# Kernel optimization log

Hardware: AMD Instinct MI355X
Metric: run time of the kernel (lower is better)

The kernel has to match this reference:

```python
import jax, jax.numpy as jnp
import numpy as np

B = 4096
FEAT = 512
EMB = 64
HID = 1024
NUM_CLASSES = 64   # == option_num == noise_lib_Y.shape[0]
LIB_X = 256
LIB_Y = 256
OUT_J = 256


def setup_inputs() -> dict:
    key = jax.random.key(0)
    ks = jax.random.split(key, 16)
    s = lambda k, shape, fan: jax.random.normal(k, shape, jnp.float32) / np.sqrt(fan)
    d_in = FEAT + EMB
    return {
        "state": jax.random.normal(ks[0], (B, FEAT), jnp.float32),
        "option": jax.random.randint(ks[1], (B,), 0, NUM_CLASSES, jnp.int64),
        "embed_table": s(ks[2], (NUM_CLASSES, EMB), EMB),
        "Wx1": s(ks[3], (d_in, HID), d_in), "bx1": jnp.zeros((HID,), jnp.float32),
        "Wx2": s(ks[4], (HID, LIB_X), HID), "bx2": jnp.zeros((LIB_X,), jnp.float32),
        "Wy1": s(ks[5], (d_in, HID), d_in), "by1": jnp.zeros((HID,), jnp.float32),
        "Wy2": s(ks[6], (HID, LIB_Y), HID), "by2": jnp.zeros((LIB_Y,), jnp.float32),
        "noise_lib_X": s(ks[7], (LIB_X, OUT_J), LIB_X),
        "noise_lib_Y": s(ks[8], (NUM_CLASSES, LIB_Y, OUT_J), LIB_Y),
    }


def _mlp(x, W1, b1, W2, b2):
    # MLP_RELU, layer_num=2: Linear -> ReLU -> Linear
    h = jax.nn.relu(x @ W1 + b1)
    return h @ W2 + b2


def reference(state, option, embed_table, Wx1, bx1, Wx2, bx2,
              Wy1, by1, Wy2, by2, noise_lib_X, noise_lib_Y):
    option_embed = embed_table[option]                      # [B, EMB]
    all_state = jnp.concatenate([state, option_embed], axis=-1)
    cls_X = _mlp(all_state, Wx1, bx1, Wx2, bx2)             # [B, LIB_X]
    cls_Y = _mlp(all_state, Wy1, by1, Wy2, by2)             # [B, LIB_Y]
    # Original: einsum('bi,mij->bmj') then mask with one_hot(option).
    # Mathematically identical gather-then-matmul (honors the routing sparsity):
    noise_Y_sel = noise_lib_Y[option]                       # [B, LIB_Y, OUT_J]
    generate_noise_Y = jnp.einsum('bi,bij->bj', cls_Y, noise_Y_sel)
    generate_noise_X = cls_X @ noise_lib_X                  # [B, OUT_J]
    return (generate_noise_X, generate_noise_Y)
```

## Files before the change

### kernel.cpp

```cpp
#include <hip/hip_runtime.h>

typedef unsigned short u16;
typedef unsigned int u32;

using f32x4  = __attribute__((ext_vector_type(4))) float;
using bf16x8 = __attribute__((ext_vector_type(8))) __bf16;

#define DEV __device__ __forceinline__

DEV u16 f2bf(float f) {
  union { float f; u32 u; } x; x.f = f;
  return (u16)((x.u + 0x7fffu + ((x.u >> 16) & 1u)) >> 16);
}
DEV float bf2f(u16 h) {
  union { u32 u; float f; } x; x.u = ((u32)h) << 16;
  return x.f;
}

DEV void async_cp16(const u16* g, u16* l) {
  __builtin_amdgcn_global_load_lds((const __attribute__((address_space(1))) void*)g,
                                   (__attribute__((address_space(3))) void*)l,
                                   16, 0, 0);
}

static constexpr int BATCH = 4096;
static constexpr int FEAT  = 512;
static constexpr int EMB   = 64;
static constexpr int HID   = 1024;
static constexpr int NC    = 64;
static constexpr int DIN   = 576;
static constexpr int LIB   = 256;

DEV void detect_lite(const u32* __restrict__ sraw, const u32* __restrict__ oraw,
                     int* isf32, int* ostr) {
  __shared__ int cib, conz;
  const int t = threadIdx.x;
  if (t == 0) { cib = 0; conz = 0; }
  u32 w = sraw[t];
  u32 e = (w >> 7) & 0xFFu;
  unsigned long long m1 = __ballot(e >= 100 && e <= 142);
  unsigned long long m2 = __ballot((t & 1) && oraw[t] != 0);
  __syncthreads();
  if ((t & 63) == 0) {
    atomicAdd(&cib, __popcll(m1));
    atomicAdd(&conz, __popcll(m2));
  }
  __syncthreads();
  *isf32 = (cib < 128) ? 1 : 0;
  *ostr  = (conz == 0) ? 2 : 1;
}

DEV void load16_bf(u16* v, const void* __restrict__ in, size_t off, int isf32) {
  if (isf32) {
    const float4* s = (const float4*)((const float*)in + off);
    float4 a0 = s[0], a1 = s[1], a2 = s[2], a3 = s[3];
    v[0] = f2bf(a0.x); v[1] = f2bf(a0.y); v[2]  = f2bf(a0.z); v[3]  = f2bf(a0.w);
    v[4] = f2bf(a1.x); v[5] = f2bf(a1.y); v[6]  = f2bf(a1.z); v[7]  = f2bf(a1.w);
    v[8] = f2bf(a2.x); v[9] = f2bf(a2.y); v[10] = f2bf(a2.z); v[11] = f2bf(a2.w);
    v[12] = f2bf(a3.x); v[13] = f2bf(a3.y); v[14] = f2bf(a3.z); v[15] = f2bf(a3.w);
  } else {
    const uint4* s = (const uint4*)((const u16*)in + off);
    *(uint4*)&v[0] = s[0];
    *(uint4*)&v[8] = s[1];
  }
}

DEV void do_transpose64(u16* lds, const void* __restrict__ in,
                        u16* __restrict__ out, int R, int C,
                        int by, int bx, int isf32) {
  u16* tile = lds;
  const int t = threadIdx.x;
  {
    const int r = t >> 2, c0 = (t & 3) * 16;
    u16 v[16];
    load16_bf(v, in, (size_t)(by * 64 + r) * C + (bx * 64 + c0), isf32);
    *(uint4*)&tile[r * 72 + c0]     = *(uint4*)&v[0];
    *(uint4*)&tile[r * 72 + c0 + 8] = *(uint4*)&v[8];
  }
  __syncthreads();
  {
    const int c = t & 63, rs = (t >> 6) * 16;
    u16 w[16];
#pragma unroll
    for (int i = 0; i < 16; ++i) w[i] = tile[(rs + i) * 72 + c];
    size_t oo = (size_t)(bx * 64 + c) * R + (by * 64 + rs);
    *(uint4*)&out[oo]     = *(uint4*)&w[0];
    *(uint4*)&out[oo + 8] = *(uint4*)&w[8];
  }
}

DEV void tgemm_task(u16* lds, const void* __restrict__ nX,
                    const void* __restrict__ Wx2, u16* __restrict__ T,
                    int mt, int nt, int isf32) {
  u16* Als = lds;
  u16* Bls = lds + 64 * 72;
  const int t = threadIdx.x;
  const int m0 = mt * 64, q0 = nt * 64;
  const int lane = t & 63, wid = t >> 6;
  const int wm = wid >> 1, wn = wid & 1;
  const int lr = lane & 15, lq = lane >> 4;
  f32x4 acc[2][2] = {};
  for (int k0 = 0; k0 < LIB; k0 += 64) {
    __syncthreads();
    {
      const int r = t >> 2, c0 = (t & 3) * 16;
      u16 v[16];
      load16_bf(v, nX, (size_t)(k0 + r) * LIB + m0 + c0, isf32);
#pragma unroll
      for (int j = 0; j < 16; ++j) Als[(c0 + j) * 72 + r] = v[j];
      const int q = t >> 2, ic = (t & 3) * 16;
      u16 w16[16];
      load16_bf(w16, Wx2, (size_t)(q0 + q) * LIB + k0 + ic, isf32);
      u16* dst = &Bls[((ic >> 5) * 64 + q) * 32 + (ic & 31)];
      *(uint4*)dst       = *(uint4*)&w16[0];
      *(uint4*)(dst + 8) = *(uint4*)&w16[8];
    }
    __syncthreads();
#pragma unroll
    for (int sl = 0; sl < 2; ++sl) {
      bf16x8 av[2], bv[2];
#pragma unroll
      for (int i2 = 0; i2 < 2; ++i2)
        av[i2] = *(const bf16x8*)&Als[(wm * 32 + i2 * 16 + lr) * 72 + sl * 32 + lq * 8];
#pragma unroll
      for (int j2 = 0; j2 < 2; ++j2)
        bv[j2] = *(const bf16x8*)&Bls[(sl * 64 + wn * 32 + j2 * 16 + lr) * 32 + lq * 8];
#pragma unroll
      for (int i2 = 0; i2 < 2; ++i2)
#pragma unroll
        for (int j2 = 0; j2 < 2; ++j2)
          acc[i2][j2] = __builtin_amdgcn_mfma_f32_16x16x32_bf16(av[i2], bv[j2], acc[i2][j2], 0, 0, 0);
    }
  }
#pragma unroll
  for (int j2 = 0; j2 < 2; ++j2) {
    const int gc = q0 + wn * 32 + j2 * 16 + lr;
#pragma unroll
    for (int i2 = 0; i2 < 2; ++i2) {
      const int gr = m0 + wm * 32 + i2 * 16 + lq * 4;
#pragma unroll
      for (int r = 0; r < 4; ++r)
        T[(size_t)(gr + r) * HID + gc] = f2bf(acc[i2][j2][r]);
    }
  }
}

struct PrepArgs {
  const void *state, *emb, *Wx1, *Wy1;
  const int* opt;
  u16 *all_state, *WT1x, *WT1y;
};
static constexpr int PB_CONCAT = BATCH * 36 / 256;
static constexpr int PB_WT1 = (DIN / 64) * (HID / 64);
static constexpr int PREP_BLOCKS = PB_CONCAT + 2 * PB_WT1;

__global__ __launch_bounds__(256) void prep_k(PrepArgs a) {
  __shared__ __align__(16) u16 plds[64 * 72];
  int isf32, os;
  detect_lite((const u32*)a.state, (const u32*)a.opt, &isf32, &os);
  int bid = blockIdx.x;
  const int t = threadIdx.x;
  if (bid < PB_CONCAT) {
    int idx = bid * 256 + t;
    int b = idx / 36, ch = idx % 36;
    const void* base;
    size_t srcoff;
    if (ch < 32) { base = a.state; srcoff = (size_t)b * FEAT + ch * 16; }
    else {
      base = a.emb;
      srcoff = (size_t)a.opt[(size_t)b * os] * EMB + (ch - 32) * 16;
    }
    u16 o[16];
    load16_bf(o, base, srcoff, isf32);
    u16* dst = a.all_state + (size_t)b * DIN + ch * 16;
    *(uint4*)dst       = *(const uint4*)&o[0];
    *(uint4*)(dst + 8) = *(const uint4*)&o[8];
    return;
  }
  bid -= PB_CONCAT;
  if (bid < PB_WT1) { do_transpose64(plds, a.Wx1, a.WT1x, DIN, HID, bid >> 4, bid & 15, isf32); return; }
  bid -= PB_WT1;
  do_transpose64(plds, a.Wy1, a.WT1y, DIN, HID, bid >> 4, bid & 15, isf32);
}

template <int BM, int BN, int SLABS, bool RELU>
DEV void gemm_tile(u16* lds, const u16* __restrict__ A, const u16* __restrict__ Bt,
                   const void* bias, void* C, int N, int K, int m0, int n0,
                   int isf32, bool cf32, bool bf32) {
  constexpr int WM = BM / 2, WN = BN / 2, TM = WM / 16, TN = WN / 16;
  u16* As = lds;
  u16* Bs = lds + BM * 32 * SLABS;
  const int t = threadIdx.x;
  const int lane = t & 63, wid = t >> 6;
  const int wm = wid >> 1, wn = wid & 1;
  const int lr = lane & 15, lq = lane >> 4;
  f32x4 acc[TM][TN] = {};
  for (int k0 = 0; k0 < K; k0 += 32 * SLABS) {
    __syncthreads();
#pragma unroll
    for (int sl = 0; sl < SLABS; ++sl) {
#pragma unroll
      for (int u = 0; u < BM / 64; ++u) {
        int unit = u * 256 + t;
        int r = unit >> 2, c8 = (unit & 3) * 8;
        async_cp16(A + (size_t)(m0 + r) * K + (k0 + sl * 32 + c8),
                   &As[(sl * BM + r) * 32 + c8]);
      }
#pragma unroll
      for (int u = 0; u < BN / 64; ++u) {
        int unit = u * 256 + t;
        int r = unit >> 2, c8 = (unit & 3) * 8;
        async_cp16(Bt + (size_t)(n0 + r) * K + (k0 + sl * 32 + c8),
                   &Bs[(sl * BN + r) * 32 + c8]);
      }
    }
    __syncthreads();
#pragma unroll
    for (int sl = 0; sl < SLABS; ++sl) {
      bf16x8 av[TM], bv[TN];
#pragma unroll
      for (int i = 0; i < TM; ++i)
        av[i] = *(const bf16x8*)&As[(sl * BM + wm * WM + i * 16 + lr) * 32 + lq * 8];
#pragma unroll
      for (int j = 0; j < TN; ++j)
        bv[j] = *(const bf16x8*)&Bs[(sl * BN + wn * WN + j * 16 + lr) * 32 + lq * 8];
#pragma unroll
      for (int i = 0; i < TM; ++i)
#pragma unroll
        for (int j = 0; j < TN; ++j)
          acc[i][j] = __builtin_amdgcn_mfma_f32_16x16x32_bf16(av[i], bv[j], acc[i][j], 0, 0, 0);
    }
  }
#pragma unroll
  for (int j = 0; j < TN; ++j) {
    const int gc = n0 + wn * WN + j * 16 + lr;
    const float bval = bias
        ? (bf32 ? ((const float*)bias)[gc] : bf2f(((const u16*)bias)[gc]))
        : 0.f;
#pragma unroll
    for (int i = 0; i < TM; ++i) {
      const int gr = m0 + wm * WM + i * 16 + lq * 4;
#pragma unroll
      for (int r = 0; r < 4; ++r) {
        float v = acc[i][j][r] + bval;
        if (RELU) v = fmaxf(v, 0.f);
        const size_t idx = (size_t)(gr + r) * N + gc;
        if (cf32) ((float*)C)[idx] = v;
        else      ((u16*)C)[idx] = f2bf(v);
      }
    }
  }
}

struct G1Args {
  const u16 *all_state, *WT1x, *WT1y;
  const void *bx1, *by1, *Wy2, *nX, *Wx2, *bx2, *state, *opt;
  u16 *h_x, *h_y, *WT2y, *T;
  float* b2x;
};
static constexpr int G1_GEMM = 1024;
static constexpr int G1_BLOCKS = G1_GEMM + 64 + 64 + 4;

__global__ __launch_bounds__(256) void gemm1_k(G1Args a) {
  __shared__ __align__(16) u16 lds[(128 + 64) * 96];
  __shared__ float red[4][64];
  int isf32, os;
  detect_lite((const u32*)a.state, (const u32*)a.opt, &isf32, &os);
  int bid = blockIdx.x;
  const int t = threadIdx.x;
  if (bid < G1_GEMM) {
    const int v = (bid & 7) * 128 + (bid >> 3);
    const int x = v & 15, y = (v >> 4) & 31, z = v >> 9;
    gemm_tile<128, 64, 3, true>(lds,
        a.all_state, z ? a.WT1y : a.WT1x, z ? a.by1 : a.bx1,
        z ? a.h_y : a.h_x, HID, DIN, y * 128, x * 64, isf32, false, isf32);
    return;
  }
  bid -= G1_GEMM;
  if (bid < 64) { do_transpose64(lds, a.Wy2, a.WT2y, HID, LIB, bid >> 2, bid & 3, isf32); return; }
  bid -= 64;
  if (bid < 64) { tgemm_task(lds, a.nX, a.Wx2, a.T, bid & 3, bid >> 2, isf32); return; }
  bid -= 64;
  {
    const int j = bid * 64 + (t & 63), g = t >> 6;
    float acc = 0.f;
    for (int ii = 0; ii < 64; ++ii) {
      const int i = g * 64 + ii;
      float s = isf32 ? ((const float*)a.bx2)[i] : bf2f(((const u16*)a.bx2)[i]);
      float v = isf32 ? ((const float*)a.nX)[(size_t)i * LIB + j]
                      : bf2f(((const u16*)a.nX)[(size_t)i * LIB + j]);
      acc += s * v;
    }
    red[g][t & 63] = acc;
    __syncthreads();
    if (g == 0)
      a.b2x[j] = red[0][t & 63] + red[1][t & 63] + red[2][t & 63] + red[3][t & 63];
  }
}

struct GArg { const u16* A; const u16* Bt; const void* bias; void* C; int cflag; int bflag; };

template <int BM, int BN, int SLABS, bool RELU>
__global__ __launch_bounds__(256) void gemm_bt(GArg g0, GArg g1, int N, int K,
                                               const void* state, const void* opt) {
  __shared__ __align__(16) u16 lds[(BM + BN) * 32 * SLABS];
  int isf32, os;
  detect_lite((const u32*)state, (const u32*)opt, &isf32, &os);
  const int cpx = gridDim.x >> 3;
  const int v = (blockIdx.x & 7) * cpx + (blockIdx.x >> 3);
  const int nx = N / BN, my = BATCH / BM;
  const int x = v % nx;
  const int rem = v / nx;
  const int y = rem % my, z = rem / my;
  const GArg g = z ? g1 : g0;
  gemm_tile<BM, BN, SLABS, RELU>(lds, g.A, g.Bt, g.bias, g.C, N, K,
                                 y * BM, x * BN,
                                 isf32, g.cflag && isf32, g.bflag || isf32);
}

struct TailArgs {
  const u16* cls_y;
  const void *nY, *state;
  const int* opt;
  void* out;
};

static constexpr int TSTR = 266;

__global__ __launch_bounds__(256) void tail_k(TailArgs a) {
  __shared__ __align__(16) u16 lds[25216];
  __shared__ int lcnt;
  int isf32, os;
  detect_lite((const u32*)a.state, (const u32*)a.opt, &isf32, &os);
  const bool of32 = (isf32 != 0);
  const int t = threadIdx.x;
  const int lane = t & 63, w = t >> 6, lr = lane & 15, lq = lane >> 4;

  u16* Bts  = lds;
  u16* Asm  = lds + 64 * TSTR;
  u16* list = lds + 80 * TSTR;
  const int v = (blockIdx.x & 7) * 64 + (blockIdx.x >> 3);
  const int m = v >> 3;
  const int n0 = ((v >> 1) & 3) * 64;
  const int half = v & 1;
  if (t == 0) lcnt = 0;

#pragma unroll
  for (int pass = 0; pass < 4; ++pass) {
    const int k = pass * 64 + (t >> 2), nc = (t & 3) * 16;
    u16 vv[16];
    load16_bf(vv, a.nY, ((size_t)m * LIB + k) * LIB + n0 + nc, isf32);
#pragma unroll
    for (int j = 0; j < 16; ++j) Bts[(nc + j) * TSTR + k] = vv[j];
  }

  __syncthreads();
  const int bstart = half * (BATCH / 2), bend = bstart + BATCH / 2;
  for (int base = bstart; base < bend; base += 256) {
    const int b = base + t;
    const int e = a.opt[(size_t)b * os];
    unsigned long long mk = __ballot(e == m);
    const int nw = __popcll(mk);
    int wbase = 0;
    if (lane == 0 && nw) wbase = atomicAdd(&lcnt, nw);
    wbase = __shfl(wbase, 0);
    const int mypre = __popcll(mk & ((1ull << lane) - 1ull));
    if (e == m) list[wbase + mypre] = (u16)b;
  }
  __syncthreads();
  const int cnt = lcnt;
  const size_t out_off = (size_t)BATCH * LIB;

  for (int ch = 0; ch < cnt; ch += 16) {
    __syncthreads();
    {
      const int r = t >> 4, cb = (t & 15) * 16;
      if (ch + r < cnt) {
        const u16* src = a.cls_y + (size_t)list[ch + r] * LIB + cb;
        *(uint4*)&Asm[r * TSTR + cb]     = *(const uint4*)src;
        *(uint4*)&Asm[r * TSTR + cb + 8] = *(const uint4*)(src + 8);
      } else {
        uint4 z{0, 0, 0, 0};
        *(uint4*)&Asm[r * TSTR + cb]     = z;
        *(uint4*)&Asm[r * TSTR + cb + 8] = z;
      }
    }
    __syncthreads();
    f32x4 acc = {};
#pragma unroll
    for (int kk = 0; kk < LIB; kk += 32) {
      bf16x8 av = *(const bf16x8*)&Asm[lr * TSTR + kk + lq * 8];
      bf16x8 bv = *(const bf16x8*)&Bts[(w * 16 + lr) * TSTR + kk + lq * 8];
      acc = __builtin_amdgcn_mfma_f32_16x16x32_bf16(av, bv, acc, 0, 0, 0);
    }
#pragma unroll
    for (int r = 0; r < 4; ++r) {
      const int rowc = lq * 4 + r;
      if (ch + rowc < cnt) {
        const size_t oi = out_off + (size_t)list[ch + rowc] * LIB
                        + (n0 + w * 16 + lr);
        if (of32) ((float*)a.out)[oi] = acc[r];
        else      ((u16*)a.out)[oi] = f2bf(acc[r]);
      }
    }
  }
}

extern "C" void kernel_launch(void* const* d_in, const int* in_sizes, int n_in,
                              void* d_out, int out_size, void* d_ws, size_t ws_size,
                              hipStream_t stream) {
  char* p = (char*)d_ws;
  auto alloc = [&](size_t bytes) { char* r = p; p += (bytes + 255) & ~(size_t)255; return r; };
  u16* all_state = (u16*)alloc((size_t)BATCH * DIN * 2);
  u16* h_x   = (u16*)alloc((size_t)BATCH * HID * 2);
  u16* h_y   = (u16*)alloc((size_t)BATCH * HID * 2);
  u16* cls_y = (u16*)alloc((size_t)BATCH * LIB * 2);
  u16* WT1x  = (u16*)alloc((size_t)HID * DIN * 2);
  u16* WT1y  = (u16*)alloc((size_t)HID * DIN * 2);
  u16* WT2y  = (u16*)alloc((size_t)LIB * HID * 2);
  u16* T     = (u16*)alloc((size_t)LIB * HID * 2);
  float* b2x = (float*)alloc((size_t)LIB * 4);

  const void* state = d_in[0];
  const void* opt   = d_in[1];

  PrepArgs pa;
  pa.state = state; pa.opt = (const int*)opt; pa.emb = d_in[2];
  pa.Wx1 = d_in[3]; pa.Wy1 = d_in[7];
  pa.all_state = all_state; pa.WT1x = WT1x; pa.WT1y = WT1y;
  prep_k<<<PREP_BLOCKS, 256, 0, stream>>>(pa);

  G1Args g1;
  g1.all_state = all_state; g1.WT1x = WT1x; g1.WT1y = WT1y;
  g1.bx1 = d_in[4]; g1.by1 = d_in[8];
  g1.Wy2 = d_in[9]; g1.nX = d_in[11]; g1.Wx2 = d_in[5]; g1.bx2 = d_in[6];
  g1.state = state; g1.opt = opt;
  g1.h_x = h_x; g1.h_y = h_y; g1.WT2y = WT2y; g1.T = T; g1.b2x = b2x;
  gemm1_k<<<G1_BLOCKS, 256, 0, stream>>>(g1);

  GArg g2x{h_x, T, b2x, d_out, 1, 1};
  GArg g2y{h_y, WT2y, d_in[10], cls_y, 0, 0};
  gemm_bt<64, 64, 4, false><<<512, 256, 0, stream>>>(
      g2x, g2y, LIB, HID, state, opt);

  TailArgs ta{cls_y, d_in[12], state, (const int*)opt, d_out};
  tail_k<<<512, 256, 0, stream>>>(ta);
}
```

Before: 151.4 us.

## Fuse all stages into one persistent kernel with grid-wide barriers

Replaces the four separate launches (prep, first GEMM, second GEMM, routed tail) with one 512-block, 512-thread kernel. The stages are separated by atomic-counter grid barriers, which are reset with a memset before launch. Each block is split into two 256-thread halves that work on independent tiles, and the first-layer GEMM slab count drops from 3 to 2. This removes inter-kernel launch gaps and drain time. In exchange it depends on all 512 blocks being co-resident to avoid deadlock, and it leaves half the threads idle in the second GEMM and tail stages.

```diff
diff --git a/kernel.cpp b/kernel.cpp
--- a/kernel.cpp
+++ b/kernel.cpp
@@ -30,6 +30,17 @@
 static constexpr int NC    = 64;
 static constexpr int DIN   = 576;
 static constexpr int LIB   = 256;
+static constexpr int NBLK  = 512;
+
+DEV void gbar(int* bar) {
+  __syncthreads();
+  if (threadIdx.x == 0) {
+    __hip_atomic_fetch_add(bar, 1, __ATOMIC_ACQ_REL, __HIP_MEMORY_SCOPE_AGENT);
+    while (__hip_atomic_load(bar, __ATOMIC_ACQUIRE, __HIP_MEMORY_SCOPE_AGENT) < NBLK)
+      __builtin_amdgcn_s_sleep(2);
+  }
+  __syncthreads();
+}
 
 DEV void detect_lite(const u32* __restrict__ sraw, const u32* __restrict__ oraw,
                      int* isf32, int* ostr) {
@@ -46,7 +57,7 @@
     atomicAdd(&conz, __popcll(m2));
   }
   __syncthreads();
-  *isf32 = (cib < 128) ? 1 : 0;
+  *isf32 = (cib < (int)(blockDim.x >> 1)) ? 1 : 0;
   *ostr  = (conz == 0) ? 2 : 1;
 }
 
@@ -65,13 +76,11 @@
   }
 }
 
-DEV void do_transpose64(u16* lds, const void* __restrict__ in,
+DEV void do_transpose64(u16* tile, const void* __restrict__ in,
                         u16* __restrict__ out, int R, int C,
-                        int by, int bx, int isf32) {
-  u16* tile = lds;
-  const int t = threadIdx.x;
-  {
-    const int r = t >> 2, c0 = (t & 3) * 16;
+                        int by, int bx, int isf32, int tt) {
+  {
+    const int r = tt >> 2, c0 = (tt & 3) * 16;
     u16 v[16];
     load16_bf(v, in, (size_t)(by * 64 + r) * C + (bx * 64 + c0), isf32);
     *(uint4*)&tile[r * 72 + c0]     = *(uint4*)&v[0];
@@ -79,7 +88,7 @@
   }
   __syncthreads();
   {
-    const int c = t & 63, rs = (t >> 6) * 16;
+    const int c = tt & 63, rs = (tt >> 6) * 16;
     u16 w[16];
 #pragma unroll
     for (int i = 0; i < 16; ++i) w[i] = tile[(rs + i) * 72 + c];
@@ -89,29 +98,27 @@
   }
 }
 
-DEV void tgemm_task(u16* lds, const void* __restrict__ nX,
+DEV void tgemm_task(u16* L, const void* __restrict__ nX,
                     const void* __restrict__ Wx2, u16* __restrict__ T,
-                    int mt, int nt, int isf32) {
-  u16* Als = lds;
-  u16* Bls = lds + 64 * 72;
-  const int t = threadIdx.x;
+                    int mt, int nt, int isf32, int tt) {
+  u16* Als = L;
+  u16* Bls = L + 64 * 72;
   const int m0 = mt * 64, q0 = nt * 64;
-  const int lane = t & 63, wid = t >> 6;
+  const int lane = tt & 63, wid = tt >> 6;
   const int wm = wid >> 1, wn = wid & 1;
   const int lr = lane & 15, lq = lane >> 4;
   f32x4 acc[2][2] = {};
   for (int k0 = 0; k0 < LIB; k0 += 64) {
     __syncthreads();
     {
-      const int r = t >> 2, c0 = (t & 3) * 16;
+      const int r = tt >> 2, c0 = (tt & 3) * 16;
       u16 v[16];
       load16_bf(v, nX, (size_t)(k0 + r) * LIB + m0 + c0, isf32);
 #pragma unroll
       for (int j = 0; j < 16; ++j) Als[(c0 + j) * 72 + r] = v[j];
-      const int q = t >> 2, ic = (t & 3) * 16;
       u16 w16[16];
-      load16_bf(w16, Wx2, (size_t)(q0 + q) * LIB + k0 + ic, isf32);
-      u16* dst = &Bls[((ic >> 5) * 64 + q) * 32 + (ic & 31)];
+      load16_bf(w16, Wx2, (size_t)(q0 + r) * LIB + k0 + c0, isf32);
+      u16* dst = &Bls[((c0 >> 5) * 64 + r) * 32 + (c0 & 31)];
       *(uint4*)dst       = *(uint4*)&w16[0];
       *(uint4*)(dst + 8) = *(uint4*)&w16[8];
     }
@@ -145,262 +152,248 @@
   }
 }
 
-struct PrepArgs {
-  const void *state, *emb, *Wx1, *Wy1;
-  const int* opt;
-  u16 *all_state, *WT1x, *WT1y;
-};
-static constexpr int PB_CONCAT = BATCH * 36 / 256;
-static constexpr int PB_WT1 = (DIN / 64) * (HID / 64);
-static constexpr int PREP_BLOCKS = PB_CONCAT + 2 * PB_WT1;
-
-__global__ __launch_bounds__(256) void prep_k(PrepArgs a) {
-  __shared__ __align__(16) u16 plds[64 * 72];
-  int isf32, os;
-  detect_lite((const u32*)a.state, (const u32*)a.opt, &isf32, &os);
-  int bid = blockIdx.x;
-  const int t = threadIdx.x;
-  if (bid < PB_CONCAT) {
-    int idx = bid * 256 + t;
-    int b = idx / 36, ch = idx % 36;
-    const void* base;
-    size_t srcoff;
-    if (ch < 32) { base = a.state; srcoff = (size_t)b * FEAT + ch * 16; }
-    else {
-      base = a.emb;
-      srcoff = (size_t)a.opt[(size_t)b * os] * EMB + (ch - 32) * 16;
-    }
-    u16 o[16];
-    load16_bf(o, base, srcoff, isf32);
-    u16* dst = a.all_state + (size_t)b * DIN + ch * 16;
-    *(uint4*)dst       = *(const uint4*)&o[0];
-    *(uint4*)(dst + 8) = *(const uint4*)&o[8];
-    return;
-  }
-  bid -= PB_CONCAT;
-  if (bid < PB_WT1) { do_transpose64(plds, a.Wx1, a.WT1x, DIN, HID, bid >> 4, bid & 15, isf32); return; }
-  bid -= PB_WT1;
-  do_transpose64(plds, a.Wy1, a.WT1y, DIN, HID, bid >> 4, bid & 15, isf32);
-}
-
 template <int BM, int BN, int SLABS, bool RELU>
-DEV void gemm_tile(u16* lds, const u16* __restrict__ A, const u16* __restrict__ Bt,
-                   const void* bias, void* C, int N, int K, int m0, int n0,
-                   int isf32, bool cf32, bool bf32) {
+DEV void gemm_tile(u16* lds, int tt, const u16* __restrict__ A,
+                   const u16* __restrict__ Bt, const void* bias, void* C,
+                   int N, int K, int m0, int n0,
+                   int isf32, bool cf32, bool bf32, bool act) {
   constexpr int WM = BM / 2, WN = BN / 2, TM = WM / 16, TN = WN / 16;
   u16* As = lds;
   u16* Bs = lds + BM * 32 * SLABS;
-  const int t = threadIdx.x;
-  const int lane = t & 63, wid = t >> 6;
+  const int lane = tt & 63, wid = tt >> 6;
   const int wm = wid >> 1, wn = wid & 1;
   const int lr = lane & 15, lq = lane >> 4;
   f32x4 acc[TM][TN] = {};
   for (int k0 = 0; k0 < K; k0 += 32 * SLABS) {
     __syncthreads();
-#pragma unroll
-    for (int sl = 0; sl < SLABS; ++sl) {
-#pragma unroll
-      for (int u = 0; u < BM / 64; ++u) {
-        int unit = u * 256 + t;
-        int r = unit >> 2, c8 = (unit & 3) * 8;
-        async_cp16(A + (size_t)(m0 + r) * K + (k0 + sl * 32 + c8),
-                   &As[(sl * BM + r) * 32 + c8]);
-      }
-#pragma unroll
-      for (int u = 0; u < BN / 64; ++u) {
-        int unit = u * 256 + t;
-        int r = unit >> 2, c8 = (unit & 3) * 8;
-        async_cp16(Bt + (size_t)(n0 + r) * K + (k0 + sl * 32 + c8),
-                   &Bs[(sl * BN + r) * 32 + c8]);
-      }
-    }
-    __syncthreads();
-#pragma unroll
-    for (int sl = 0; sl < SLABS; ++sl) {
-      bf16x8 av[TM], bv[TN];
-#pragma unroll
-      for (int i = 0; i < TM; ++i)
-        av[i] = *(const bf16x8*)&As[(sl * BM + wm * WM + i * 16 + lr) * 32 + lq * 8];
-#pragma unroll
-      for (int j = 0; j < TN; ++j)
-        bv[j] = *(const bf16x8*)&Bs[(sl * BN + wn * WN + j * 16 + lr) * 32 + lq * 8];
-#pragma unroll
-      for (int i = 0; i < TM; ++i)
+    if (act) {
+#pragma unroll
+      for (int sl = 0; sl < SLABS; ++sl) {
+#pragma unroll
+        for (int u = 0; u < BM / 64; ++u) {
+          int unit = u * 256 + tt;
+          int r = unit >> 2, c8 = (unit & 3) * 8;
+          async_cp16(A + (size_t)(m0 + r) * K + (k0 + sl * 32 + c8),
+                     &As[(sl * BM + r) * 32 + c8]);
+        }
+#pragma unroll
+        for (int u = 0; u < BN / 64; ++u) {
+          int unit = u * 256 + tt;
+          int r = unit >> 2, c8 = (unit & 3) * 8;
+          async_cp16(Bt + (size_t)(n0 + r) * K + (k0 + sl * 32 + c8),
+                     &Bs[(sl * BN + r) * 32 + c8]);
+        }
+      }
+    }
+    __syncthreads();
+    if (act) {
+#pragma unroll
+      for (int sl = 0; sl < SLABS; ++sl) {
+        bf16x8 av[TM], bv[TN];
+#pragma unroll
+        for (int i = 0; i < TM; ++i)
+          av[i] = *(const bf16x8*)&As[(sl * BM + wm * WM + i * 16 + lr) * 32 + lq * 8];
 #pragma unroll
         for (int j = 0; j < TN; ++j)
-          acc[i][j] = __builtin_amdgcn_mfma_f32_16x16x32_bf16(av[i], bv[j], acc[i][j], 0, 0, 0);
-    }
-  }
-#pragma unroll
-  for (int j = 0; j < TN; ++j) {
-    const int gc = n0 + wn * WN + j * 16 + lr;
-    const float bval = bias
-        ? (bf32 ? ((const float*)bias)[gc] : bf2f(((const u16*)bias)[gc]))
-        : 0.f;
-#pragma unroll
-    for (int i = 0; i < TM; ++i) {
-      const int gr = m0 + wm * WM + i * 16 + lq * 4;
-#pragma unroll
-      for (int r = 0; r < 4; ++r) {
-        float v = acc[i][j][r] + bval;
-        if (RELU) v = fmaxf(v, 0.f);
-        const size_t idx = (size_t)(gr + r) * N + gc;
-        if (cf32) ((float*)C)[idx] = v;
-        else      ((u16*)C)[idx] = f2bf(v);
-      }
-    }
-  }
-}
-
-struct G1Args {
-  const u16 *all_state, *WT1x, *WT1y;
-  const void *bx1, *by1, *Wy2, *nX, *Wx2, *bx2, *state, *opt;
-  u16 *h_x, *h_y, *WT2y, *T;
+          bv[j] = *(const bf16x8*)&Bs[(sl * BN + wn * WN + j * 16 + lr) * 32 + lq * 8];
+#pragma unroll
+        for (int i = 0; i < TM; ++i)
+#pragma unroll
+          for (int j = 0; j < TN; ++j)
+            acc[i][j] = __builtin_amdgcn_mfma_f32_16x16x32_bf16(av[i], bv[j], acc[i][j], 0, 0, 0);
+      }
+    }
+  }
+  if (act) {
+#pragma unroll
+    for (int j = 0; j < TN; ++j) {
+      const int gc = n0 + wn * WN + j * 16 + lr;
+      const float bval = bias
+          ? (bf32 ? ((const float*)bias)[gc] : bf2f(((const u16*)bias)[gc]))
+          : 0.f;
+#pragma unroll
+      for (int i = 0; i < TM; ++i) {
+        const int gr = m0 + wm * WM + i * 16 + lq * 4;
+#pragma unroll
+        for (int r = 0; r < 4; ++r) {
+          float v = acc[i][j][r] + bval;
+          if (RELU) v = fmaxf(v, 0.f);
+          const size_t idx = (size_t)(gr + r) * N + gc;
+          if (cf32) ((float*)C)[idx] = v;
+          else      ((u16*)C)[idx] = f2bf(v);
+        }
+      }
+    }
+  }
+}
+
+struct FArgs {
+  const void *state, *emb, *Wx1, *bx1, *Wx2, *bx2, *Wy1, *by1, *Wy2, *by2, *nX, *nY;
+  const int* opt;
+  u16 *all_state, *h_x, *h_y, *cls_y, *WT1x, *WT1y, *WT2y, *T;
   float* b2x;
+  void* out;
+  int* bar;
 };
-static constexpr int G1_GEMM = 1024;
-static constexpr int G1_BLOCKS = G1_GEMM + 64 + 64 + 4;
-
-__global__ __launch_bounds__(256) void gemm1_k(G1Args a) {
-  __shared__ __align__(16) u16 lds[(128 + 64) * 96];
-  __shared__ float red[4][64];
-  int isf32, os;
-  detect_lite((const u32*)a.state, (const u32*)a.opt, &isf32, &os);
-  int bid = blockIdx.x;
-  const int t = threadIdx.x;
-  if (bid < G1_GEMM) {
-    const int v = (bid & 7) * 128 + (bid >> 3);
-    const int x = v & 15, y = (v >> 4) & 31, z = v >> 9;
-    gemm_tile<128, 64, 3, true>(lds,
-        a.all_state, z ? a.WT1y : a.WT1x, z ? a.by1 : a.bx1,
-        z ? a.h_y : a.h_x, HID, DIN, y * 128, x * 64, isf32, false, isf32);
-    return;
-  }
-  bid -= G1_GEMM;
-  if (bid < 64) { do_transpose64(lds, a.Wy2, a.WT2y, HID, LIB, bid >> 2, bid & 3, isf32); return; }
-  bid -= 64;
-  if (bid < 64) { tgemm_task(lds, a.nX, a.Wx2, a.T, bid & 3, bid >> 2, isf32); return; }
-  bid -= 64;
-  {
-    const int j = bid * 64 + (t & 63), g = t >> 6;
-    float acc = 0.f;
-    for (int ii = 0; ii < 64; ++ii) {
-      const int i = g * 64 + ii;
-      float s = isf32 ? ((const float*)a.bx2)[i] : bf2f(((const u16*)a.bx2)[i]);
-      float v = isf32 ? ((const float*)a.nX)[(size_t)i * LIB + j]
-                      : bf2f(((const u16*)a.nX)[(size_t)i * LIB + j]);
-      acc += s * v;
-    }
-    red[g][t & 63] = acc;
-    __syncthreads();
-    if (g == 0)
-      a.b2x[j] = red[0][t & 63] + red[1][t & 63] + red[2][t & 63] + red[3][t & 63];
-  }
-}
-
-struct GArg { const u16* A; const u16* Bt; const void* bias; void* C; int cflag; int bflag; };
-
-template <int BM, int BN, int SLABS, bool RELU>
-__global__ __launch_bounds__(256) void gemm_bt(GArg g0, GArg g1, int N, int K,
-                                               const void* state, const void* opt) {
-  __shared__ __align__(16) u16 lds[(BM + BN) * 32 * SLABS];
-  int isf32, os;
-  detect_lite((const u32*)state, (const u32*)opt, &isf32, &os);
-  const int cpx = gridDim.x >> 3;
-  const int v = (blockIdx.x & 7) * cpx + (blockIdx.x >> 3);
-  const int nx = N / BN, my = BATCH / BM;
-  const int x = v % nx;
-  const int rem = v / nx;
-  const int y = rem % my, z = rem / my;
-  const GArg g = z ? g1 : g0;
-  gemm_tile<BM, BN, SLABS, RELU>(lds, g.A, g.Bt, g.bias, g.C, N, K,
-                                 y * BM, x * BN,
-                                 isf32, g.cflag && isf32, g.bflag || isf32);
-}
-
-struct TailArgs {
-  const u16* cls_y;
-  const void *nY, *state;
-  const int* opt;
-  void* out;
-};
 
 static constexpr int TSTR = 266;
 
-__global__ __launch_bounds__(256) void tail_k(TailArgs a) {
+__global__ __launch_bounds__(512, 4) void fused_k(FArgs a) {
   __shared__ __align__(16) u16 lds[25216];
   __shared__ int lcnt;
   int isf32, os;
   detect_lite((const u32*)a.state, (const u32*)a.opt, &isf32, &os);
-  const bool of32 = (isf32 != 0);
+  const int bid = blockIdx.x;
   const int t = threadIdx.x;
-  const int lane = t & 63, w = t >> 6, lr = lane & 15, lq = lane >> 4;
-
-  u16* Bts  = lds;
-  u16* Asm  = lds + 64 * TSTR;
-  u16* list = lds + 80 * TSTR;
-  const int v = (blockIdx.x & 7) * 64 + (blockIdx.x >> 3);
-  const int m = v >> 3;
-  const int n0 = ((v >> 1) & 3) * 64;
-  const int half = v & 1;
-  if (t == 0) lcnt = 0;
-
-#pragma unroll
-  for (int pass = 0; pass < 4; ++pass) {
-    const int k = pass * 64 + (t >> 2), nc = (t & 3) * 16;
-    u16 vv[16];
-    load16_bf(vv, a.nY, ((size_t)m * LIB + k) * LIB + n0 + nc, isf32);
-#pragma unroll
-    for (int j = 0; j < 16; ++j) Bts[(nc + j) * TSTR + k] = vv[j];
-  }
-
-  __syncthreads();
-  const int bstart = half * (BATCH / 2), bend = bstart + BATCH / 2;
-  for (int base = bstart; base < bend; base += 256) {
-    const int b = base + t;
-    const int e = a.opt[(size_t)b * os];
-    unsigned long long mk = __ballot(e == m);
-    const int nw = __popcll(mk);
-    int wbase = 0;
-    if (lane == 0 && nw) wbase = atomicAdd(&lcnt, nw);
-    wbase = __shfl(wbase, 0);
-    const int mypre = __popcll(mk & ((1ull << lane) - 1ull));
-    if (e == m) list[wbase + mypre] = (u16)b;
-  }
-  __syncthreads();
-  const int cnt = lcnt;
-  const size_t out_off = (size_t)BATCH * LIB;
-
-  for (int ch = 0; ch < cnt; ch += 16) {
-    __syncthreads();
-    {
-      const int r = t >> 4, cb = (t & 15) * 16;
-      if (ch + r < cnt) {
-        const u16* src = a.cls_y + (size_t)list[ch + r] * LIB + cb;
-        *(uint4*)&Asm[r * TSTR + cb]     = *(const uint4*)src;
-        *(uint4*)&Asm[r * TSTR + cb + 8] = *(const uint4*)(src + 8);
-      } else {
-        uint4 z{0, 0, 0, 0};
-        *(uint4*)&Asm[r * TSTR + cb]     = z;
-        *(uint4*)&Asm[r * TSTR + cb + 8] = z;
-      }
-    }
-    __syncthreads();
-    f32x4 acc = {};
-#pragma unroll
-    for (int kk = 0; kk < LIB; kk += 32) {
-      bf16x8 av = *(const bf16x8*)&Asm[lr * TSTR + kk + lq * 8];
-      bf16x8 bv = *(const bf16x8*)&Bts[(w * 16 + lr) * TSTR + kk + lq * 8];
-      acc = __builtin_amdgcn_mfma_f32_16x16x32_bf16(av, bv, acc, 0, 0, 0);
-    }
-#pragma unroll
-    for (int r = 0; r < 4; ++r) {
-      const int rowc = lq * 4 + r;
-      if (ch + rowc < cnt) {
-        const size_t oi = out_off + (size_t)list[ch + rowc] * LIB
-                        + (n0 + w * 16 + lr);
-        if (of32) ((float*)a.out)[oi] = acc[r];
-        else      ((u16*)a.out)[oi] = f2bf(acc[r]);
+  const int half = t >> 8, tt = t & 255;
+
+  {
+    const int u = bid * 2 + half;
+    u16* L = lds + half * 8704;
+    if (u < 576) {
+      int idx = u * 256 + tt;
+      int b = idx / 36, ch = idx % 36;
+      const void* base;
+      size_t srcoff;
+      if (ch < 32) { base = a.state; srcoff = (size_t)b * FEAT + ch * 16; }
+      else {
+        base = a.emb;
+        srcoff = (size_t)a.opt[(size_t)b * os] * EMB + (ch - 32) * 16;
+      }
+      u16 o[16];
+      load16_bf(o, base, srcoff, isf32);
+      u16* dst = a.all_state + (size_t)b * DIN + ch * 16;
+      *(uint4*)dst       = *(const uint4*)&o[0];
+      *(uint4*)(dst + 8) = *(const uint4*)&o[8];
+    } else if (u < 720) {
+      const int v = u - 576;
+      do_transpose64(L, a.Wx1, a.WT1x, DIN, HID, v >> 4, v & 15, isf32, tt);
+    } else if (u < 864) {
+      const int v = u - 720;
+      do_transpose64(L, a.Wy1, a.WT1y, DIN, HID, v >> 4, v & 15, isf32, tt);
+    } else if (u < 928) {
+      const int v = u - 864;
+      do_transpose64(L, a.Wy2, a.WT2y, HID, LIB, v >> 2, v & 3, isf32, tt);
+    } else if (u < 992) {
+      const int v = u - 928;
+      tgemm_task(L, a.nX, a.Wx2, a.T, v & 3, v >> 2, isf32, tt);
+    } else if (u < 996) {
+      float* red = (float*)L;
+      const int j = (u - 992) * 64 + (tt & 63), g = tt >> 6;
+      float acc = 0.f;
+      for (int ii = 0; ii < 64; ++ii) {
+        const int i = g * 64 + ii;
+        float s = isf32 ? ((const float*)a.bx2)[i] : bf2f(((const u16*)a.bx2)[i]);
+        float v = isf32 ? ((const float*)a.nX)[(size_t)i * LIB + j]
+                        : bf2f(((const u16*)a.nX)[(size_t)i * LIB + j]);
+        acc += s * v;
+      }
+      red[g * 64 + (tt & 63)] = acc;
+      __syncthreads();
+      if (g == 0)
+        a.b2x[j] = red[tt & 63] + red[64 + (tt & 63)] +
+                   red[128 + (tt & 63)] + red[192 + (tt & 63)];
+    }
+  }
+  gbar(a.bar + 0);
+
+  {
+    const int v = bid * 2 + half;
+    const int x = v & 15, y = (v >> 4) & 31, z = v >> 9;
+    gemm_tile<128, 64, 2, true>(lds + half * 12288, tt,
+        a.all_state, z ? a.WT1y : a.WT1x, z ? a.by1 : a.bx1,
+        z ? a.h_y : a.h_x, HID, DIN, y * 128, x * 64, isf32, false,
+        isf32 != 0, true);
+  }
+  gbar(a.bar + 1);
+
+  {
+    const int x = bid & 3, y = (bid >> 2) & 63, z = bid >> 8;
+    const u16* A2   = z ? a.h_y : a.h_x;
+    const u16* Bt2  = z ? a.WT2y : a.T;
+    const void* bi2 = z ? a.by2 : (const void*)a.b2x;
+    void* C2        = z ? (void*)a.cls_y : a.out;
+    const bool cf2  = (!z) && isf32;
+    const bool bf2  = z ? (isf32 != 0) : true;
+    gemm_tile<64, 64, 4, false>(lds, tt, A2, Bt2, bi2, C2, LIB, HID,
+                                y * 64, x * 64, isf32, cf2, bf2, half == 0);
+  }
+  gbar(a.bar + 2);
+
+  {
+    const bool act = (half == 0);
+    const bool of32 = (isf32 != 0);
+    const int lane = tt & 63, w = tt >> 6, lr = lane & 15, lq = lane >> 4;
+    u16* Bts  = lds;
+    u16* Asm  = lds + 64 * TSTR;
+    u16* list = lds + 80 * TSTR;
+    const int m = bid >> 3;
+    const int n0 = ((bid >> 1) & 3) * 64;
+    const int bh = bid & 1;
+    if (t == 0) lcnt = 0;
+
+    if (act) {
+#pragma unroll
+      for (int pass = 0; pass < 4; ++pass) {
+        const int k = pass * 64 + (tt >> 2), nc = (tt & 3) * 16;
+        u16 v[16];
+        load16_bf(v, a.nY, ((size_t)m * LIB + k) * LIB + n0 + nc, isf32);
+#pragma unroll
+        for (int j = 0; j < 16; ++j) Bts[(nc + j) * TSTR + k] = v[j];
+      }
+    }
+    __syncthreads();
+    if (act) {
+      const int bstart = bh * (BATCH / 2), bend = bstart + BATCH / 2;
+      for (int base = bstart; base < bend; base += 256) {
+        const int b = base + tt;
+        const int e = a.opt[(size_t)b * os];
+        unsigned long long mk = __ballot(e == m);
+        const int nw = __popcll(mk);
+        int wbase = 0;
+        if (lane == 0 && nw) wbase = atomicAdd(&lcnt, nw);
+        wbase = __shfl(wbase, 0);
+        const int mypre = __popcll(mk & ((1ull << lane) - 1ull));
+        if (e == m) list[wbase + mypre] = (u16)b;
+      }
+    }
+    __syncthreads();
+    const int cnt = lcnt;
+    const size_t out_off = (size_t)BATCH * LIB;
+
+    for (int ch = 0; ch < cnt; ch += 16) {
+      __syncthreads();
+      if (act) {
+        const int r = tt >> 4, cb = (tt & 15) * 16;
+        if (ch + r < cnt) {
+          const u16* src = a.cls_y + (size_t)list[ch + r] * LIB + cb;
+          *(uint4*)&Asm[r * TSTR + cb]     = *(const uint4*)src;
+          *(uint4*)&Asm[r * TSTR + cb + 8] = *(const uint4*)(src + 8);
+        } else {
+          uint4 z4{0, 0, 0, 0};
+          *(uint4*)&Asm[r * TSTR + cb]     = z4;
+          *(uint4*)&Asm[r * TSTR + cb + 8] = z4;
+        }
+      }
+      __syncthreads();
+      if (act) {
+        f32x4 acc = {};
+#pragma unroll
+        for (int kk = 0; kk < LIB; kk += 32) {
+          bf16x8 av = *(const bf16x8*)&Asm[lr * TSTR + kk + lq * 8];
+          bf16x8 bv = *(const bf16x8*)&Bts[(w * 16 + lr) * TSTR + kk + lq * 8];
+          acc = __builtin_amdgcn_mfma_f32_16x16x32_bf16(av, bv, acc, 0, 0, 0);
+        }
+#pragma unroll
+        for (int r = 0; r < 4; ++r) {
+          const int rowc = lq * 4 + r;
+          if (ch + rowc < cnt) {
+            const size_t oi = out_off + (size_t)list[ch + rowc] * LIB
+                            + (n0 + w * 16 + lr);
+            if (of32) ((float*)a.out)[oi] = acc[r];
+            else      ((u16*)a.out)[oi] = f2bf(acc[r]);
+          }
+        }
       }
     }
   }
@@ -411,6 +404,7 @@
                               hipStream_t stream) {
   char* p = (char*)d_ws;
   auto alloc = [&](size_t bytes) { char* r = p; p += (bytes + 255) & ~(size_t)255; return r; };
+  int* bar = (int*)alloc(3 * sizeof(int));
   u16* all_state = (u16*)alloc((size_t)BATCH * DIN * 2);
   u16* h_x   = (u16*)alloc((size_t)BATCH * HID * 2);
   u16* h_y   = (u16*)alloc((size_t)BATCH * HID * 2);
@@ -421,28 +415,16 @@
   u16* T     = (u16*)alloc((size_t)LIB * HID * 2);
   float* b2x = (float*)alloc((size_t)LIB * 4);
 
-  const void* state = d_in[0];
-  const void* opt   = d_in[1];
-
-  PrepArgs pa;
-  pa.state = state; pa.opt = (const int*)opt; pa.emb = d_in[2];
-  pa.Wx1 = d_in[3]; pa.Wy1 = d_in[7];
-  pa.all_state = all_state; pa.WT1x = WT1x; pa.WT1y = WT1y;
-  prep_k<<<PREP_BLOCKS, 256, 0, stream>>>(pa);
-
-  G1Args g1;
-  g1.all_state = all_state; g1.WT1x = WT1x; g1.WT1y = WT1y;
-  g1.bx1 = d_in[4]; g1.by1 = d_in[8];
-  g1.Wy2 = d_in[9]; g1.nX = d_in[11]; g1.Wx2 = d_in[5]; g1.bx2 = d_in[6];
-  g1.state = state; g1.opt = opt;
-  g1.h_x = h_x; g1.h_y = h_y; g1.WT2y = WT2y; g1.T = T; g1.b2x = b2x;
-  gemm1_k<<<G1_BLOCKS, 256, 0, stream>>>(g1);
-
-  GArg g2x{h_x, T, b2x, d_out, 1, 1};
-  GArg g2y{h_y, WT2y, d_in[10], cls_y, 0, 0};
-  gemm_bt<64, 64, 4, false><<<512, 256, 0, stream>>>(
-      g2x, g2y, LIB, HID, state, opt);
-
-  TailArgs ta{cls_y, d_in[12], state, (const int*)opt, d_out};
-  tail_k<<<512, 256, 0, stream>>>(ta);
-}
+  hipMemsetAsync(bar, 0, 3 * sizeof(int), stream);
+
+  FArgs fa;
+  fa.state = d_in[0]; fa.opt = (const int*)d_in[1]; fa.emb = d_in[2];
+  fa.Wx1 = d_in[3]; fa.bx1 = d_in[4]; fa.Wx2 = d_in[5]; fa.bx2 = d_in[6];
+  fa.Wy1 = d_in[7]; fa.by1 = d_in[8]; fa.Wy2 = d_in[9]; fa.by2 = d_in[10];
+  fa.nX = d_in[11]; fa.nY = d_in[12];
+  fa.all_state = all_state; fa.h_x = h_x; fa.h_y = h_y; fa.cls_y = cls_y;
+  fa.WT1x = WT1x; fa.WT1y = WT1y; fa.WT2y = WT2y; fa.T = T; fa.b2x = b2x;
+  fa.out = d_out; fa.bar = bar;
+
+  fused_k<<<NBLK, 512, 0, stream>>>(fa);
+}
```

Measured after the change: 336.2 us. 2.22x slower.
